# Kernel optimization log

Measured on AMD Instinct MI355X. Metric: run time of the kernel, lower is better.

Reference implementation:

```python
import jax, jax.numpy as jnp
import numpy as np

A = 256       # number of nodes (node_vec.shape[0])
F = 256       # dim_feature
C = 32        # dim_outerproduct
EPS = 1e-5    # NORM_SMALL


def setup_inputs() -> dict:
    key = jax.random.key(0)
    ks = jax.random.split(key, 8)
    inp = {
        "node_vec": jax.random.normal(ks[0], (A, F), dtype=jnp.float32),
        "node_mask": jnp.ones((A,), dtype=jnp.float32),
        "ln_scale": jnp.ones((F,), dtype=jnp.float32),
        "ln_bias": jnp.zeros((F,), dtype=jnp.float32),
        "Wl": jax.random.normal(ks[1], (F, C), dtype=jnp.float32) / np.sqrt(F),
        "bl": jnp.zeros((C,), dtype=jnp.float32),
        "Wr": jax.random.normal(ks[2], (F, C), dtype=jnp.float32) / np.sqrt(F),
        "br": jnp.zeros((C,), dtype=jnp.float32),
        "Wo": jax.random.normal(ks[3], (C * C, F), dtype=jnp.float32) / np.sqrt(C * C),
        "bo": jnp.zeros((F,), dtype=jnp.float32),
    }
    return inp


def reference(node_vec, node_mask, ln_scale, ln_bias, Wl, bl, Wr, br, Wo, bo):
    # LayerNorm over the feature axis
    mu = jnp.mean(node_vec, axis=-1, keepdims=True)
    var = jnp.mean(jnp.square(node_vec - mu), axis=-1, keepdims=True)
    act = (node_vec - mu) * jax.lax.rsqrt(var + EPS) * ln_scale + ln_bias

    # Dual projections, masked per node
    left_act = (act @ Wl + bl) * node_mask[:, None]    # [A, C]
    right_act = (act @ Wr + br) * node_mask[:, None]   # [A, C]

    # Explicit outer product. Original computes a [C*A, A*C] matmul then
    # reshapes/transposes to [A, A, C*C]; equivalently:
    # out4[a, b, c, d] = left_act[a, c] * right_act[b, d]
    out_act = jnp.einsum('ac,bd->abcd', left_act, right_act)  # [A, A, C, C]
    out_act = out_act.reshape((node_vec.shape[0], node_vec.shape[0], C * C))

    # Output projection
    return out_act @ Wo + bo  # [A, A, F]
```

## Files before the change

kernel.cpp:

```cpp
#include <hip/hip_runtime.h>

#define A_N 256
#define F_N 256
#define C_N 32

__global__ __launch_bounds__(256) void ln_proj_kernel(
    const float* __restrict__ node_vec, const float* __restrict__ node_mask,
    const float* __restrict__ ln_scale, const float* __restrict__ ln_bias,
    const float* __restrict__ Wl, const float* __restrict__ bl,
    const float* __restrict__ Wr, const float* __restrict__ br,
    float* __restrict__ left, float* __restrict__ right) {
  const int a = blockIdx.x;
  const int t = threadIdx.x;
  __shared__ float sAct[F_N];
  __shared__ float sRed[8];
  __shared__ float sPl[8][C_N];
  __shared__ float sPr[8][C_N];

  float x = node_vec[a * F_N + t];

  float s = x;
  for (int off = 32; off; off >>= 1) s += __shfl_down(s, off, 64);
  const int wave = t >> 6, lane = t & 63;
  if (lane == 0) sRed[wave] = s;
  __syncthreads();
  if (t == 0) sRed[4] = (sRed[0] + sRed[1] + sRed[2] + sRed[3]) * (1.0f / F_N);
  __syncthreads();
  const float mu = sRed[4];
  const float d = x - mu;

  s = d * d;
  for (int off = 32; off; off >>= 1) s += __shfl_down(s, off, 64);
  if (lane == 0) sRed[wave] = s;
  __syncthreads();
  if (t == 0) {
    float v = (sRed[0] + sRed[1] + sRed[2] + sRed[3]) * (1.0f / F_N);
    sRed[5] = rsqrtf(v + 1e-5f);
  }
  __syncthreads();
  const float act = d * sRed[5] * ln_scale[t] + ln_bias[t];
  sAct[t] = act;
  __syncthreads();

  const int c = t & 31, seg = t >> 5;
  float pl = 0.f, pr = 0.f;
  const float* actp = &sAct[seg * 32];
#pragma unroll
  for (int j = 0; j < 32; ++j) {
    const float av = actp[j];
    const int widx = (seg * 32 + j) * C_N + c;
    pl = fmaf(av, Wl[widx], pl);
    pr = fmaf(av, Wr[widx], pr);
  }
  sPl[seg][c] = pl;
  sPr[seg][c] = pr;
  __syncthreads();
  if (t < C_N) {
    const float m = node_mask[a];
    float suml = bl[t], sumr = br[t];
#pragma unroll
    for (int sg = 0; sg < 8; ++sg) { suml += sPl[sg][t]; sumr += sPr[sg][t]; }
    left[a * C_N + t] = suml * m;
    right[a * C_N + t] = sumr * m;
  }
}

__global__ __launch_bounds__(256) void compT_kernel(
    const float* __restrict__ right, const float* __restrict__ Wo,
    float* __restrict__ T) {
  const int c = blockIdx.y;
  const int b0 = blockIdx.x * 16;
  const int f = threadIdx.x;
  __shared__ float sWo[C_N * F_N];
  __shared__ float sR[16 * C_N];

#pragma unroll
  for (int d = 0; d < C_N; ++d)
    sWo[d * F_N + f] = Wo[(c * C_N + d) * F_N + f];
  sR[f] = right[b0 * C_N + f];
  sR[256 + f] = right[b0 * C_N + 256 + f];
  __syncthreads();

  float acc[16];
#pragma unroll
  for (int b = 0; b < 16; ++b) acc[b] = 0.f;

#pragma unroll
  for (int d = 0; d < C_N; ++d) {
    const float wv = sWo[d * F_N + f];
#pragma unroll
    for (int b = 0; b < 16; ++b)
      acc[b] = fmaf(sR[b * C_N + d], wv, acc[b]);
  }

#pragma unroll
  for (int b = 0; b < 16; ++b)
    T[(size_t)(b0 + b) * (C_N * F_N) + c * F_N + f] = acc[b];
}

__global__ __launch_bounds__(256) void out_kernel(
    const float* __restrict__ left, const float* __restrict__ T,
    const float* __restrict__ bo, float* __restrict__ out) {
  const int b = blockIdx.y;
  const int a0 = blockIdx.x * 64;
  const int t = threadIdx.x;
  const int fq = t & 63;
  const int arow = t >> 6;

  __shared__ float sT[C_N * F_N];
  __shared__ float sL[64 * C_N];

  float4* sT4 = (float4*)sT;
  const float4* Tg4 = (const float4*)(T + (size_t)b * (C_N * F_N));
#pragma unroll
  for (int k = 0; k < 8; ++k) sT4[k * 256 + t] = Tg4[k * 256 + t];
  float4* sL4 = (float4*)sL;
  const float4* Lg4 = (const float4*)(left + a0 * C_N);
#pragma unroll
  for (int k = 0; k < 2; ++k) sL4[k * 256 + t] = Lg4[k * 256 + t];
  const float4 bias4 = ((const float4*)bo)[fq];
  __syncthreads();

  float4 acc[16];
#pragma unroll
  for (int i = 0; i < 16; ++i) acc[i] = bias4;

  const float* sLrow = &sL[(arow * 16) * C_N];
#pragma unroll 8
  for (int c = 0; c < C_N; ++c) {
    const float4 tv = sT4[c * 64 + fq];
#pragma unroll
    for (int i = 0; i < 16; ++i) {
      const float lv = sLrow[i * C_N + c];
      acc[i].x = fmaf(lv, tv.x, acc[i].x);
      acc[i].y = fmaf(lv, tv.y, acc[i].y);
      acc[i].z = fmaf(lv, tv.z, acc[i].z);
      acc[i].w = fmaf(lv, tv.w, acc[i].w);
    }
  }

  float4* out4 = (float4*)out;
  const size_t rowq = (size_t)(A_N * F_N) / 4;
#pragma unroll
  for (int i = 0; i < 16; ++i)
    out4[(size_t)(a0 + arow * 16 + i) * rowq + (size_t)b * 64 + fq] = acc[i];
}

extern "C" void kernel_launch(void* const* d_in, const int* in_sizes, int n_in,
                              void* d_out, int out_size, void* d_ws, size_t ws_size,
                              hipStream_t stream) {
  const float* node_vec  = (const float*)d_in[0];
  const float* node_mask = (const float*)d_in[1];
  const float* ln_scale  = (const float*)d_in[2];
  const float* ln_bias   = (const float*)d_in[3];
  const float* Wl        = (const float*)d_in[4];
  const float* bl        = (const float*)d_in[5];
  const float* Wr        = (const float*)d_in[6];
  const float* br        = (const float*)d_in[7];
  const float* Wo        = (const float*)d_in[8];
  const float* bo        = (const float*)d_in[9];
  float* out = (float*)d_out;

  float* left  = (float*)d_ws;
  float* right = left + A_N * C_N;
  float* T     = right + A_N * C_N;

  ln_proj_kernel<<<A_N, 256, 0, stream>>>(node_vec, node_mask, ln_scale, ln_bias,
                                          Wl, bl, Wr, br, left, right);
  compT_kernel<<<dim3(16, 32), 256, 0, stream>>>(right, Wo, T);
  out_kernel<<<dim3(4, A_N), 256, 0, stream>>>(left, T, bo, out);
}
```

Baseline: 114.7 us.

## Use bf16 MFMA for output projection with bf16 left and pre-swizzled T

The left activations and the intermediate T (right contracted with Wo) are now stored in bf16. T is written in a layout matching MFMA B-fragments. The output kernel uses 16x16x32 bf16 MFMA instructions instead of scalar FP32 FMAs, and compT is rewritten to read Wo directly without shared memory. The goal is to cut compute time and halve intermediate traffic. The cost is bf16 rounding error in the output and scattered 4-byte output stores.

Result: slower. 156.4 us (+36.3%).

```diff
diff --git a/kernel.cpp b/kernel.cpp
--- a/kernel.cpp
+++ b/kernel.cpp
@@ -4,12 +4,22 @@
 #define F_N 256
 #define C_N 32
 
+typedef __attribute__((ext_vector_type(8))) short bf16x8;
+typedef __attribute__((ext_vector_type(4))) float f32x4;
+typedef __attribute__((ext_vector_type(8))) unsigned short ushort8;
+
+__device__ __forceinline__ unsigned short f2bf(float x) {
+  union { float f; unsigned u; } v; v.f = x;
+  unsigned r = v.u + 0x7FFF + ((v.u >> 16) & 1);
+  return (unsigned short)(r >> 16);
+}
+
 __global__ __launch_bounds__(256) void ln_proj_kernel(
     const float* __restrict__ node_vec, const float* __restrict__ node_mask,
     const float* __restrict__ ln_scale, const float* __restrict__ ln_bias,
     const float* __restrict__ Wl, const float* __restrict__ bl,
     const float* __restrict__ Wr, const float* __restrict__ br,
-    float* __restrict__ left, float* __restrict__ right) {
+    unsigned short* __restrict__ leftbf, float* __restrict__ right) {
   const int a = blockIdx.x;
   const int t = threadIdx.x;
   __shared__ float sAct[F_N];
@@ -60,90 +70,97 @@
     float suml = bl[t], sumr = br[t];
 #pragma unroll
     for (int sg = 0; sg < 8; ++sg) { suml += sPl[sg][t]; sumr += sPr[sg][t]; }
-    left[a * C_N + t] = suml * m;
+    leftbf[a * C_N + t] = f2bf(suml * m);
     right[a * C_N + t] = sumr * m;
   }
 }
 
 __global__ __launch_bounds__(256) void compT_kernel(
     const float* __restrict__ right, const float* __restrict__ Wo,
-    float* __restrict__ T) {
-  const int c = blockIdx.y;
-  const int b0 = blockIdx.x * 16;
-  const int f = threadIdx.x;
-  __shared__ float sWo[C_N * F_N];
-  __shared__ float sR[16 * C_N];
+    unsigned short* __restrict__ T2) {
+  const int b = blockIdx.x;
+  const int t = threadIdx.x;
+  const int fq = t & 63;
+  const int cq = t >> 6;
 
+  float rv[C_N];
 #pragma unroll
-  for (int d = 0; d < C_N; ++d)
-    sWo[d * F_N + f] = Wo[(c * C_N + d) * F_N + f];
-  sR[f] = right[b0 * C_N + f];
-  sR[256 + f] = right[b0 * C_N + 256 + f];
-  __syncthreads();
+  for (int d = 0; d < C_N; ++d) rv[d] = right[b * C_N + d];
 
-  float acc[16];
+  const f32x4* Wo4 = (const f32x4*)Wo;
+  f32x4 acc[8];
 #pragma unroll
-  for (int b = 0; b < 16; ++b) acc[b] = 0.f;
+  for (int ci = 0; ci < 8; ++ci) acc[ci] = (f32x4){0.f, 0.f, 0.f, 0.f};
 
 #pragma unroll
   for (int d = 0; d < C_N; ++d) {
-    const float wv = sWo[d * F_N + f];
 #pragma unroll
-    for (int b = 0; b < 16; ++b)
-      acc[b] = fmaf(sR[b * C_N + d], wv, acc[b]);
-  }
-
-#pragma unroll
-  for (int b = 0; b < 16; ++b)
-    T[(size_t)(b0 + b) * (C_N * F_N) + c * F_N + f] = acc[b];
-}
-
-__global__ __launch_bounds__(256) void out_kernel(
-    const float* __restrict__ left, const float* __restrict__ T,
-    const float* __restrict__ bo, float* __restrict__ out) {
-  const int b = blockIdx.y;
-  const int a0 = blockIdx.x * 64;
-  const int t = threadIdx.x;
-  const int fq = t & 63;
-  const int arow = t >> 6;
-
-  __shared__ float sT[C_N * F_N];
-  __shared__ float sL[64 * C_N];
-
-  float4* sT4 = (float4*)sT;
-  const float4* Tg4 = (const float4*)(T + (size_t)b * (C_N * F_N));
-#pragma unroll
-  for (int k = 0; k < 8; ++k) sT4[k * 256 + t] = Tg4[k * 256 + t];
-  float4* sL4 = (float4*)sL;
-  const float4* Lg4 = (const float4*)(left + a0 * C_N);
-#pragma unroll
-  for (int k = 0; k < 2; ++k) sL4[k * 256 + t] = Lg4[k * 256 + t];
-  const float4 bias4 = ((const float4*)bo)[fq];
-  __syncthreads();
-
-  float4 acc[16];
-#pragma unroll
-  for (int i = 0; i < 16; ++i) acc[i] = bias4;
-
-  const float* sLrow = &sL[(arow * 16) * C_N];
-#pragma unroll 8
-  for (int c = 0; c < C_N; ++c) {
-    const float4 tv = sT4[c * 64 + fq];
-#pragma unroll
-    for (int i = 0; i < 16; ++i) {
-      const float lv = sLrow[i * C_N + c];
-      acc[i].x = fmaf(lv, tv.x, acc[i].x);
-      acc[i].y = fmaf(lv, tv.y, acc[i].y);
-      acc[i].z = fmaf(lv, tv.z, acc[i].z);
-      acc[i].w = fmaf(lv, tv.w, acc[i].w);
+    for (int ci = 0; ci < 8; ++ci) {
+      const f32x4 w = Wo4[(size_t)((8 * cq + ci) * C_N + d) * 64 + fq];
+      acc[ci] += rv[d] * w;
     }
   }
 
-  float4* out4 = (float4*)out;
-  const size_t rowq = (size_t)(A_N * F_N) / 4;
+  const int ft = fq >> 2;
+  ushort8* T8 = (ushort8*)T2;
 #pragma unroll
-  for (int i = 0; i < 16; ++i)
-    out4[(size_t)(a0 + arow * 16 + i) * rowq + (size_t)b * 64 + fq] = acc[i];
+  for (int q = 0; q < 4; ++q) {
+    const int l = cq * 16 + 4 * (fq & 3) + q;
+    ushort8 o;
+#pragma unroll
+    for (int ci = 0; ci < 8; ++ci) o[ci] = f2bf(acc[ci][q]);
+    T8[(size_t)(b * 16 + ft) * 64 + l] = o;
+  }
+}
+
+__global__ __launch_bounds__(256) void out_mfma_kernel(
+    const unsigned short* __restrict__ leftbf,
+    const unsigned short* __restrict__ T2,
+    const float* __restrict__ bo, float* __restrict__ out) {
+  const int ah = blockIdx.x;
+  const int b = blockIdx.y;
+  const int t = threadIdx.x;
+  const int w = t >> 6;
+  const int l = t & 63;
+  const int lr = l & 15;
+  const int lk = l >> 4;
+
+  bf16x8 afrag[8];
+#pragma unroll
+  for (int m = 0; m < 8; ++m) {
+    const int a = ah * 128 + m * 16 + lr;
+    afrag[m] = *(const bf16x8*)(leftbf + a * C_N + lk * 8);
+  }
+
+  bf16x8 bfrag[4];
+  float bv[4];
+#pragma unroll
+  for (int q = 0; q < 4; ++q) {
+    const int ft = w * 4 + q;
+    bfrag[q] = *(const bf16x8*)(T2 + ((size_t)(b * 16 + ft) * 64 + l) * 8);
+    bv[q] = bo[ft * 16 + lr];
+  }
+
+  const size_t rowstride = (size_t)A_N * F_N;
+#pragma unroll
+  for (int q = 0; q < 4; ++q) {
+    const int ft = w * 4 + q;
+    const int col = b * F_N + ft * 16 + lr;
+    f32x4 acc[8];
+#pragma unroll
+    for (int m = 0; m < 8; ++m)
+      acc[m] = (f32x4){bv[q], bv[q], bv[q], bv[q]};
+#pragma unroll
+    for (int m = 0; m < 8; ++m)
+      acc[m] = __builtin_amdgcn_mfma_f32_16x16x32_bf16(afrag[m], bfrag[q], acc[m], 0, 0, 0);
+#pragma unroll
+    for (int m = 0; m < 8; ++m) {
+      const int arow = ah * 128 + m * 16 + lk * 4;
+#pragma unroll
+      for (int i = 0; i < 4; ++i)
+        out[(size_t)(arow + i) * rowstride + col] = acc[m][i];
+    }
+  }
 }
 
 extern "C" void kernel_launch(void* const* d_in, const int* in_sizes, int n_in,
@@ -161,12 +178,12 @@
   const float* bo        = (const float*)d_in[9];
   float* out = (float*)d_out;
 
-  float* left  = (float*)d_ws;
-  float* right = left + A_N * C_N;
-  float* T     = right + A_N * C_N;
+  float* right           = (float*)d_ws;
+  unsigned short* leftbf = (unsigned short*)(right + A_N * C_N);
+  unsigned short* T2     = (unsigned short*)((char*)d_ws + 65536);
 
   ln_proj_kernel<<<A_N, 256, 0, stream>>>(node_vec, node_mask, ln_scale, ln_bias,
-                                          Wl, bl, Wr, br, left, right);
-  compT_kernel<<<dim3(16, 32), 256, 0, stream>>>(right, Wo, T);
-  out_kernel<<<dim3(4, A_N), 256, 0, stream>>>(left, T, bo, out);
+                                          Wl, bl, Wr, br, leftbf, right);
+  compT_kernel<<<A_N, 256, 0, stream>>>(right, Wo, T2);
+  out_mfma_kernel<<<dim3(2, A_N), 256, 0, stream>>>(leftbf, T2, bo, out);
 }
```
